# Kernel tuning notes

Hardware: AMD Instinct MI355X
Metric: run time of the kernel (lower is better)

The kernel has to match this reference:

```python
import jax, jax.numpy as jnp
import numpy as np

N_A, N_B = 50000, 20000   # authors, teams
E0, E1, E2 = 600000, 300000, 300000  # coauthor(A->A), writes(A->B), influences(B->A)
D = 128                   # in_feats = out_feats


def setup_inputs() -> dict:
    key = jax.random.key(0)
    ks = jax.random.split(key, 12)
    h_A = jax.random.normal(ks[0], (N_A, D), jnp.float32)
    h_B = jax.random.normal(ks[1], (N_B, D), jnp.float32)
    W0 = jax.random.normal(ks[2], (D, D), jnp.float32) * 0.05
    W1 = jax.random.normal(ks[3], (D, D), jnp.float32) * 0.05
    W2 = jax.random.normal(ks[4], (D, D), jnp.float32) * 0.05
    b0 = jnp.zeros((D,), jnp.float32)
    b1 = jnp.zeros((D,), jnp.float32)
    b2 = jnp.zeros((D,), jnp.float32)
    src0 = jax.random.randint(ks[5], (E0,), 0, N_A)
    dst0 = jax.random.randint(ks[6], (E0,), 0, N_A)
    src1 = jax.random.randint(ks[7], (E1,), 0, N_A)
    dst1 = jax.random.randint(ks[8], (E1,), 0, N_B)
    src2 = jax.random.randint(ks[9], (E2,), 0, N_B)
    dst2 = jax.random.randint(ks[10], (E2,), 0, N_A)
    return dict(h_A=h_A, h_B=h_B, W0=W0, b0=b0, W1=W1, b1=b1, W2=W2, b2=b2,
                src0=src0, dst0=dst0, src1=src1, dst1=dst1, src2=src2, dst2=dst2)


def _graph_conv(x_src, W, b, src, dst, n_dst):
    """DGL GraphConv, norm='both': out = D_dst^{-1/2} A D_src^{-1/2} (X W) + b."""
    n_src = x_src.shape[0]
    ones = jnp.ones(src.shape[0], x_src.dtype)
    deg_out = jnp.clip(jax.ops.segment_sum(ones, src, num_segments=n_src), 1.0)
    deg_in = jnp.clip(jax.ops.segment_sum(ones, dst, num_segments=n_dst), 1.0)
    m = (x_src @ W) * (deg_out ** -0.5)[:, None]          # [n_src, D]
    agg = jax.ops.segment_sum(m[src], dst, num_segments=n_dst)  # [n_dst, D]
    return agg * (deg_in ** -0.5)[:, None] + b


def reference(h_A, h_B, W0, b0, W1, b1, W2, b2, src0, dst0, src1, dst1, src2, dst2):
    # HeteroGraphConv(aggregate='sum'): sum per-relation GraphConv outputs per dst ntype.
    out_A = (_graph_conv(h_A, W0, b0, src0, dst0, N_A)
             + _graph_conv(h_B, W2, b2, src2, dst2, N_A))
    out_B = _graph_conv(h_A, W1, b1, src1, dst1, N_B)
    # every ntype present in h receives an output, so no passthrough branch fires
    return out_A, out_B
```

## Files before the change

kernel.cpp:

```cpp
#include <hip/hip_runtime.h>

#define NA 50000
#define NB 20000
#define NE0 600000
#define NE1 300000
#define NE2 300000
#define DD 128
#define SUB 32768
#define PER 18750
#define PSUB 8192


typedef short bf16x8 __attribute__((ext_vector_type(8)));
typedef float f32x4 __attribute__((ext_vector_type(4)));

__device__ __forceinline__ unsigned short f2bf(float f) {
    union { float f; unsigned int u; } v; v.f = f;
    unsigned int r = v.u + 0x7fffu + ((v.u >> 16) & 1u);
    return (unsigned short)(r >> 16);
}
__device__ __forceinline__ float lo2f(unsigned int u) {
    union { float f; unsigned int u; } v; v.u = u << 16;
    return v.f;
}
__device__ __forceinline__ float hi2f(unsigned int u) {
    union { float f; unsigned int u; } v; v.u = u & 0xffff0000u;
    return v.f;
}

__global__ __launch_bounds__(1024) void hist_kernel(
    const int* __restrict__ s0, const int* __restrict__ d0,
    const int* __restrict__ s1, const int* __restrict__ d1,
    const int* __restrict__ s2, const int* __restrict__ d2,
    unsigned int* __restrict__ Pd,
    const float* __restrict__ W0, const float* __restrict__ W1,
    const float* __restrict__ W2, unsigned short* __restrict__ Wt)
{
    __shared__ unsigned int h32[SUB / 2];
    const int cfg = blockIdx.z;
    if (cfg == 6) {
        int flat = blockIdx.y * 2 + blockIdx.x;
        if (flat >= 48) return;
        int i = flat * 1024 + threadIdx.x;
        int w = i >> 14, r = i & (DD * DD - 1);
        int c = r >> 7, k = r & (DD - 1);
        const float* W = (w == 0) ? W0 : ((w == 1) ? W1 : W2);
        Wt[i] = f2bf(W[k * DD + c]);
        return;
    }
    const int En[6] = {NE0, NE0, NE1, NE1, NE2, NE2};
    const int Kn[6] = {NA, NA, NA, NB, NB, NA};
    const int Gn[6] = {32, 32, 16, 16, 16, 16};
    const int Po[6] = {0, 1600000, 3200000, 4000000, 4320000, 4640000};
    int E = En[cfg], K = Kn[cfg], G = Gn[cfg];
    int sub = blockIdx.x, g = blockIdx.y;
    int nsub = (K + SUB - 1) / SUB;
    if (sub >= nsub || g >= G) return;
    const int* keys = cfg == 0 ? s0 : cfg == 1 ? d0 : cfg == 2 ? s1
                    : cfg == 3 ? d1 : cfg == 4 ? s2 : d2;
    int lo = sub * SUB;
    int hi = min(K, lo + SUB);
    int cnt = hi - lo;
    for (int i = threadIdx.x; i < SUB / 2; i += 1024) h32[i] = 0;
    __syncthreads();
    int e1 = min(E, g * PER + PER);
    for (int e = g * PER + threadIdx.x; e < e1; e += 1024) {
        int k = keys[e];
        if (k >= lo && k < hi) {
            int kk = k - lo;
            atomicAdd(&h32[kk >> 1], 1u << ((kk & 1) << 4));
        }
    }
    __syncthreads();
    unsigned int* outp = Pd + ((Po[cfg] + g * K + lo) >> 1);
    for (int i = threadIdx.x; i < cnt / 2; i += 1024) outp[i] = h32[i];
}

__global__ __launch_bounds__(256) void reduce2(
    const unsigned short* __restrict__ P16, int* __restrict__ ideg,
    float* __restrict__ rdeg, int* __restrict__ spart,
    unsigned char* __restrict__ cum8)
{
    __shared__ int lds[256];
    const int y = blockIdx.y;
    const int Ro[6] = {0, NA, 2 * NA, 3 * NA, 3 * NA + NB, 3 * NA + 2 * NB};
    const int Kr[6] = {NA, NA, NA, NB, NB, NA};
    const int Gr[6] = {32, 32, 16, 16, 16, 16};
    const int Po[6] = {0, 1600000, 3200000, 4000000, 4320000, 4640000};
    const int Co[6] = {0, 0, 0, 1600000, 0, 1920000};
    int K = Kr[y], G = Gr[y];
    int b = blockIdx.x, t = threadIdx.x;
    int nchunk = (K + 255) >> 8;
    if (b >= nchunk) return;
    int key = b * 256 + t;
    bool valid = key < K;
    bool din = (y == 1) || (y == 3) || (y == 5);
    const unsigned short* p = P16 + Po[y] + key;
    unsigned char* cb = cum8 + Co[y] + key;
    int run = 0;
    for (int g = 0; g < G; ++g) {
        if (din && valid) cb[g * K] = (unsigned char)run;
        run += valid ? p[g * K] : 0;
    }
    if (valid) {
        ideg[Ro[y] + key] = run;
        rdeg[Ro[y] + key] = rsqrtf(fmaxf((float)run, 1.f));
    }
    if (din) {
        int slot = (y - 1) >> 1;
        lds[t] = run; __syncthreads();
        for (int o = 128; o > 0; o >>= 1) {
            if (t < o) lds[t] += lds[t + o];
            __syncthreads();
        }
        if (t == 0) spart[slot * 256 + b] = lds[0];
    }
}

__global__ __launch_bounds__(256) void scan3(
    const int* __restrict__ ideg, const int* __restrict__ spart,
    int* __restrict__ rp)
{
    __shared__ int lds[256];
    const int y = blockIdx.y;
    const int off[3] = {NA, 3 * NA, 3 * NA + 2 * NB};
    const int nn[3]  = {NA, NB, NA};
    const int ro[3]  = {0, NA, NA + NB};
    int n = nn[y];
    int b = blockIdx.x, t = threadIdx.x;
    if (b * 1024 >= n) return;

    lds[t] = (t < 4 * b) ? spart[y * 256 + t] : 0;
    __syncthreads();
    for (int o = 128; o > 0; o >>= 1) {
        if (t < o) lds[t] += lds[t + o];
        __syncthreads();
    }
    int pv = lds[0];
    __syncthreads();

    const int* deg = ideg + off[y];
    int base = b * 1024 + t * 4;
    int v[4]; int tsum = 0;
    #pragma unroll
    for (int k = 0; k < 4; ++k) {
        v[k] = (base + k < n) ? deg[base + k] : 0;
        tsum += v[k];
    }
    lds[t] = tsum; __syncthreads();
    for (int o = 1; o < 256; o <<= 1) {
        int x = (t >= o) ? lds[t - o] : 0;
        __syncthreads();
        lds[t] += x;
        __syncthreads();
    }
    int run = lds[t] - tsum + pv;
    int* rowptr = rp + ro[y];
    #pragma unroll
    for (int k = 0; k < 4; ++k) {
        if (base + k < n) rowptr[base + k] = run;
        run += v[k];
    }
}

__global__ __launch_bounds__(512) void work_kernel(
    const int* __restrict__ s0, const int* __restrict__ d0,
    const int* __restrict__ s1, const int* __restrict__ d1,
    const int* __restrict__ s2, const int* __restrict__ d2,
    const unsigned char* __restrict__ cum8, const int* __restrict__ rp,
    unsigned short* __restrict__ csr0, unsigned short* __restrict__ csr1,
    unsigned short* __restrict__ csr2,
    const float* __restrict__ hA, const float* __restrict__ hB,
    const unsigned short* __restrict__ Wt, const float* __restrict__ rdeg,
    unsigned short* __restrict__ mA0, unsigned short* __restrict__ mA1,
    unsigned short* __restrict__ mB2)
{
    __shared__ int cnt_lds[PSUB];
    int bx = blockIdx.x;
    int wid  = threadIdx.x >> 6;
    int lane = threadIdx.x & 63;
    int quad = lane >> 4;
    int l16  = lane & 15;
    if (bx < 391) {
        int base = bx * 128 + wid * 16;
        if (base >= NA) return;
        int arow = base + l16;
        if (arow >= NA) arow = NA - 1;
        bf16x8 a[4];
        #pragma unroll
        for (int kk = 0; kk < 4; ++kk) {
            const float4* p = (const float4*)(hA + (size_t)arow * DD + kk * 32 + quad * 8);
            float4 u = p[0], w = p[1];
            bf16x8 t;
            t[0] = (short)f2bf(u.x); t[1] = (short)f2bf(u.y);
            t[2] = (short)f2bf(u.z); t[3] = (short)f2bf(u.w);
            t[4] = (short)f2bf(w.x); t[5] = (short)f2bf(w.y);
            t[6] = (short)f2bf(w.z); t[7] = (short)f2bf(w.w);
            a[kk] = t;
        }
        float rs0[4], rs1[4]; int orow0 = base + quad * 4;
        #pragma unroll
        for (int r = 0; r < 4; ++r) {
            int orow = orow0 + r; int c = orow < NA ? orow : 0;
            rs0[r] = rdeg[c]; rs1[r] = rdeg[2 * NA + c];
        }
        #pragma unroll
        for (int ct = 0; ct < 8; ++ct) {
            f32x4 acc0 = {0.f, 0.f, 0.f, 0.f};
            f32x4 acc1 = {0.f, 0.f, 0.f, 0.f};
            const unsigned short* wp = Wt + (size_t)(ct * 16 + l16) * DD + quad * 8;
            #pragma unroll
            for (int kk = 0; kk < 4; ++kk) {
                bf16x8 b0 = *(const bf16x8*)(wp + kk * 32);
                bf16x8 b1 = *(const bf16x8*)(wp + 16384 + kk * 32);
                acc0 = __builtin_amdgcn_mfma_f32_16x16x32_bf16(a[kk], b0, acc0, 0, 0, 0);
                acc1 = __builtin_amdgcn_mfma_f32_16x16x32_bf16(a[kk], b1, acc1, 0, 0, 0);
            }
            #pragma unroll
            for (int r = 0; r < 4; ++r) {
                int orow = orow0 + r;
                if (orow < NA) {
                    mA0[(size_t)orow * DD + ct * 16 + l16] = f2bf(acc0[r] * rs0[r]);
                    mA1[(size_t)orow * DD + ct * 16 + l16] = f2bf(acc1[r] * rs1[r]);
                }
            }
        }
        return;
    }
    if (bx < 548) {
        int base = (bx - 391) * 128 + wid * 16;
        if (base >= NB) return;
        int arow = base + l16;
        if (arow >= NB) arow = NB - 1;
        bf16x8 a[4];
        #pragma unroll
        for (int kk = 0; kk < 4; ++kk) {
            const float4* p = (const float4*)(hB + (size_t)arow * DD + kk * 32 + quad * 8);
            float4 u = p[0], w = p[1];
            bf16x8 t;
            t[0] = (short)f2bf(u.x); t[1] = (short)f2bf(u.y);
            t[2] = (short)f2bf(u.z); t[3] = (short)f2bf(u.w);
            t[4] = (short)f2bf(w.x); t[5] = (short)f2bf(w.y);
            t[6] = (short)f2bf(w.z); t[7] = (short)f2bf(w.w);
            a[kk] = t;
        }
        float rs[4]; int orow0 = base + quad * 4;
        #pragma unroll
        for (int r = 0; r < 4; ++r) {
            int orow = orow0 + r;
            rs[r] = rdeg[3 * NA + NB + (orow < NB ? orow : 0)];
        }
        #pragma unroll
        for (int ct = 0; ct < 8; ++ct) {
            f32x4 acc = {0.f, 0.f, 0.f, 0.f};
            const unsigned short* wp = Wt + 32768 + (size_t)(ct * 16 + l16) * DD + quad * 8;
            #pragma unroll
            for (int kk = 0; kk < 4; ++kk) {
                bf16x8 b = *(const bf16x8*)(wp + kk * 32);
                acc = __builtin_amdgcn_mfma_f32_16x16x32_bf16(a[kk], b, acc, 0, 0, 0);
            }
            #pragma unroll
            for (int r = 0; r < 4; ++r) {
                int orow = orow0 + r;
                if (orow < NB)
                    mB2[(size_t)orow * DD + ct * 16 + l16] = f2bf(acc[r] * rs[r]);
            }
        }
        return;
    }
    int pb = bx - 548;
    int z, g, sub;
    if (pb < 224)      { z = 0; g = pb / 7;          sub = pb % 7; }
    else if (pb < 272) { z = 1; g = (pb - 224) / 3;  sub = (pb - 224) % 3; }
    else               { z = 2; g = (pb - 272) / 7;  sub = (pb - 272) % 7; }
    const int En[3] = {NE0, NE1, NE2};
    const int Kn[3] = {NA, NB, NA};
    const int Co[3] = {0, 1600000, 1920000};
    const int ro[3] = {0, NA, NA + NB};
    int E = En[z], K = Kn[z];
    const int* src = z == 0 ? s0 : z == 1 ? s1 : s2;
    const int* dst = z == 0 ? d0 : z == 1 ? d1 : d2;
    unsigned short* csr = z == 0 ? csr0 : z == 1 ? csr1 : csr2;
    int lo = sub * PSUB;
    int hi = min(K, lo + PSUB);
    int cnt = hi - lo;
    const int* rpz = rp + ro[z] + lo;
    const unsigned char* cz = cum8 + Co[z] + (size_t)g * K + lo;
    for (int i = threadIdx.x; i < cnt; i += 512)
        cnt_lds[i] = rpz[i] + (int)cz[i];
    __syncthreads();
    int e1 = min(E, g * PER + PER);
    for (int e = g * PER + threadIdx.x; e < e1; e += 512) {
        int d = dst[e];
        if (d >= lo && d < hi) {
            int pos = atomicAdd(&cnt_lds[d - lo], 1);
            csr[pos] = (unsigned short)src[e];
        }
    }
}

__device__ __forceinline__ void acc8(float* o, uint4 u) {
    o[0] += lo2f(u.x); o[1] += hi2f(u.x);
    o[2] += lo2f(u.y); o[3] += hi2f(u.y);
    o[4] += lo2f(u.z); o[5] += hi2f(u.z);
    o[6] += lo2f(u.w); o[7] += hi2f(u.w);
}
__device__ __forceinline__ void gather_rel4(
    const char* __restrict__ Mb, const unsigned short* __restrict__ csr,
    int st, int n, int lane, int q, unsigned laneoff, float* o)
{
    for (int ch = 0; ch < n; ch += 64) {
        int m = n - ch; if (m > 64) m = 64;
        int idx = csr[st + ch + (lane < m ? lane : m - 1)];
        int j = 0;
        for (; j + 8 <= m; j += 8) {
            int sA = __shfl(idx, j + q);
            int sB = __shfl(idx, j + 4 + q);
            uint4 uA = *(const uint4*)(Mb + (((unsigned)sA << 8) + laneoff));
            uint4 uB = *(const uint4*)(Mb + (((unsigned)sB << 8) + laneoff));
            acc8(o, uA); acc8(o, uB);
        }
        if (j + 4 <= m) {
            int s = __shfl(idx, j + q);
            uint4 u = *(const uint4*)(Mb + (((unsigned)s << 8) + laneoff));
            acc8(o, u);
            j += 4;
        }
        if (j < m) {
            int jj = j + q;
            float w = jj < m ? 1.f : 0.f;
            int s = __shfl(idx, jj < m ? jj : m - 1);
            uint4 u = *(const uint4*)(Mb + (((unsigned)s << 8) + laneoff));
            o[0] = fmaf(w, lo2f(u.x), o[0]); o[1] = fmaf(w, hi2f(u.x), o[1]);
            o[2] = fmaf(w, lo2f(u.y), o[2]); o[3] = fmaf(w, hi2f(u.y), o[3]);
            o[4] = fmaf(w, lo2f(u.z), o[4]); o[5] = fmaf(w, hi2f(u.z), o[5]);
            o[6] = fmaf(w, lo2f(u.w), o[6]); o[7] = fmaf(w, hi2f(u.w), o[7]);
        }
    }
}

__global__ __launch_bounds__(256) void gather_all(
    const unsigned short* __restrict__ mA0, const unsigned short* __restrict__ mA1,
    const unsigned short* __restrict__ mB2,
    const unsigned short* __restrict__ csr0, const unsigned short* __restrict__ csr1,
    const unsigned short* __restrict__ csr2,
    const int* __restrict__ rp, const int* __restrict__ ideg,
    const float* __restrict__ rdeg,
    const float* __restrict__ b0, const float* __restrict__ b1,
    const float* __restrict__ b2,
    float* __restrict__ out)
{
    int wid = threadIdx.x >> 6, lane = threadIdx.x & 63;
    int q = lane >> 4, l16 = lane & 15;
    unsigned laneoff = (unsigned)l16 * 16u;
    float v[8];
    #pragma unroll
    for (int i = 0; i < 8; ++i) v[i] = 0.f;
    float* op;
    const float *bia, *bib;

    if (blockIdx.x < 12500) {
        int d = blockIdx.x * 4 + wid;
        float c[8];
        #pragma unroll
        for (int i = 0; i < 8; ++i) c[i] = 0.f;
        gather_rel4((const char*)mA0, csr0, rp[d], ideg[NA + d], lane, q, laneoff, v);
        gather_rel4((const char*)mB2, csr2, rp[NA + NB + d], ideg[3 * NA + 2 * NB + d],
                    lane, q, laneoff, c);
        float r0 = rdeg[NA + d], r2 = rdeg[3 * NA + 2 * NB + d];
        #pragma unroll
        for (int i = 0; i < 8; ++i) v[i] = v[i] * r0 + c[i] * r2;
        op = out + (size_t)d * DD;
        bia = b0; bib = b2;
    } else {
        int d = (blockIdx.x - 12500) * 4 + wid;
        gather_rel4((const char*)mA1, csr1, rp[NA + d], ideg[3 * NA + d],
                    lane, q, laneoff, v);
        float r1 = rdeg[3 * NA + d];
        #pragma unroll
        for (int i = 0; i < 8; ++i) v[i] *= r1;
        op = out + (size_t)(NA + d) * DD;
        bia = b1; bib = 0;
    }

    #pragma unroll
    for (int i = 0; i < 8; ++i) {
        v[i] += __shfl_down(v[i], 32);
        v[i] += __shfl_down(v[i], 16);
    }
    if (lane < 16) {
        int col = l16 * 8;
        float4 ba0 = *(const float4*)(bia + col);
        float4 ba1 = *(const float4*)(bia + col + 4);
        if (bib) {
            float4 bb0 = *(const float4*)(bib + col);
            float4 bb1 = *(const float4*)(bib + col + 4);
            ba0.x += bb0.x; ba0.y += bb0.y; ba0.z += bb0.z; ba0.w += bb0.w;
            ba1.x += bb1.x; ba1.y += bb1.y; ba1.z += bb1.z; ba1.w += bb1.w;
        }
        float4 o0 = {v[0] + ba0.x, v[1] + ba0.y, v[2] + ba0.z, v[3] + ba0.w};
        float4 o1 = {v[4] + ba1.x, v[5] + ba1.y, v[6] + ba1.z, v[7] + ba1.w};
        *(float4*)(op + col) = o0;
        *(float4*)(op + col + 4) = o1;
    }
}

extern "C" void kernel_launch(void* const* d_in, const int* in_sizes, int n_in,
                              void* d_out, int out_size, void* d_ws, size_t ws_size,
                              hipStream_t stream) {
    const float* hA = (const float*)d_in[0];
    const float* hB = (const float*)d_in[1];
    const float* W0 = (const float*)d_in[2];
    const float* b0 = (const float*)d_in[3];
    const float* W1 = (const float*)d_in[4];
    const float* b1 = (const float*)d_in[5];
    const float* W2 = (const float*)d_in[6];
    const float* b2 = (const float*)d_in[7];
    const int* s0 = (const int*)d_in[8];
    const int* d0 = (const int*)d_in[9];
    const int* s1 = (const int*)d_in[10];
    const int* d1 = (const int*)d_in[11];
    const int* s2 = (const int*)d_in[12];
    const int* d2 = (const int*)d_in[13];
    float* out = (float*)d_out;
    char* ws = (char*)d_ws;

    unsigned short* mA0 = (unsigned short*)(ws + 0);
    unsigned short* mA1 = (unsigned short*)(ws + 12800000);
    unsigned short* mB2 = (unsigned short*)(ws + 25600000);
    unsigned short* P16 = (unsigned short*)(ws + 0);
    unsigned int*   Pd  = (unsigned int*)(ws + 0);
    unsigned short* Wt  = (unsigned short*)(ws + 30720000);
    float* rdeg         = (float*)(ws + 30818304);
    int*   ideg         = (int*)  (ws + 31778304);
    int*   rp           = (int*)  (ws + 32738304);
    int*   spart        = (int*)  (ws + 33218304);
    unsigned char* cum8 = (unsigned char*)(ws + 33221376);
    unsigned short* csr0= (unsigned short*)(ws + 35941376);
    unsigned short* csr1= (unsigned short*)(ws + 37141376);
    unsigned short* csr2= (unsigned short*)(ws + 37741376);

    hist_kernel<<<dim3(2, 32, 7), 1024, 0, stream>>>(s0, d0, s1, d1, s2, d2,
        Pd, W0, W1, W2, Wt);
    reduce2<<<dim3(196, 6), 256, 0, stream>>>(P16, ideg, rdeg, spart, cum8);
    scan3<<<dim3(49, 3), 256, 0, stream>>>(ideg, spart, rp);
    work_kernel<<<548 + 384, 512, 0, stream>>>(s0, d0, s1, d1, s2, d2,
        cum8, rp, csr0, csr1, csr2,
        hA, hB, Wt, rdeg, mA0, mA1, mB2);
    gather_all<<<12500 + 5000, 256, 0, stream>>>(mA0, mA1, mB2,
        csr0, csr1, csr2, rp, ideg, rdeg, b0, b1, b2, out);
}
```

Measured before the change: 243.1 us.

## Build degrees and CSR with global atomics instead of LDS partial histograms

Replaces the LDS-privatized partial histograms and the per-group cumulative offset table (hist_kernel, reduce2, cum8) with direct global atomicAdd degree counting over all edges, after a small zeroing kernel. The CSR fill now takes a per-row cursor, initialised from the row pointers in scan3, and claims slots with global atomics. This removes the repeated edge scans per key subrange and the large partial-count buffers. In exchange it relies on global atomic throughput and makes the order of neighbours within each CSR row nondeterministic.

```diff
diff --git a/kernel.cpp b/kernel.cpp
--- a/kernel.cpp
+++ b/kernel.cpp
@@ -6,9 +6,6 @@
 #define NE1 300000
 #define NE2 300000
 #define DD 128
-#define SUB 32768
-#define PER 18750
-#define PSUB 8192
 
 
 typedef short bf16x8 __attribute__((ext_vector_type(8)));
@@ -28,98 +25,79 @@
     return v.f;
 }
 
-__global__ __launch_bounds__(1024) void hist_kernel(
+__global__ __launch_bounds__(1024) void zero_k(int4* __restrict__ idegv)
+{
+    int i = blockIdx.x * 1024 + threadIdx.x;
+    if (i < 60000) { int4 z = {0, 0, 0, 0}; idegv[i] = z; }
+}
+
+__global__ __launch_bounds__(1024) void degwt_k(
     const int* __restrict__ s0, const int* __restrict__ d0,
     const int* __restrict__ s1, const int* __restrict__ d1,
     const int* __restrict__ s2, const int* __restrict__ d2,
-    unsigned int* __restrict__ Pd,
+    int* __restrict__ ideg,
     const float* __restrict__ W0, const float* __restrict__ W1,
     const float* __restrict__ W2, unsigned short* __restrict__ Wt)
 {
-    __shared__ unsigned int h32[SUB / 2];
-    const int cfg = blockIdx.z;
-    if (cfg == 6) {
-        int flat = blockIdx.y * 2 + blockIdx.x;
-        if (flat >= 48) return;
-        int i = flat * 1024 + threadIdx.x;
+    int bx = blockIdx.x;
+    if (bx < 48) {
+        int i = bx * 1024 + threadIdx.x;
         int w = i >> 14, r = i & (DD * DD - 1);
         int c = r >> 7, k = r & (DD - 1);
         const float* W = (w == 0) ? W0 : ((w == 1) ? W1 : W2);
         Wt[i] = f2bf(W[k * DD + c]);
         return;
     }
-    const int En[6] = {NE0, NE0, NE1, NE1, NE2, NE2};
-    const int Kn[6] = {NA, NA, NA, NB, NB, NA};
-    const int Gn[6] = {32, 32, 16, 16, 16, 16};
-    const int Po[6] = {0, 1600000, 3200000, 4000000, 4320000, 4640000};
-    int E = En[cfg], K = Kn[cfg], G = Gn[cfg];
-    int sub = blockIdx.x, g = blockIdx.y;
-    int nsub = (K + SUB - 1) / SUB;
-    if (sub >= nsub || g >= G) return;
-    const int* keys = cfg == 0 ? s0 : cfg == 1 ? d0 : cfg == 2 ? s1
-                    : cfg == 3 ? d1 : cfg == 4 ? s2 : d2;
-    int lo = sub * SUB;
-    int hi = min(K, lo + SUB);
-    int cnt = hi - lo;
-    for (int i = threadIdx.x; i < SUB / 2; i += 1024) h32[i] = 0;
+    int pb = bx - 48;
+    int z = (pb < 293) ? 0 : (pb < 440) ? 1 : 2;
+    const int zb[3] = {0, 293, 440};
+    const int En[3] = {NE0, NE1, NE2};
+    const int so[3] = {0, 2 * NA, 3 * NA + NB};
+    const int di[3] = {NA, 3 * NA, 3 * NA + 2 * NB};
+    int E = En[z];
+    const int* src = z == 0 ? s0 : z == 1 ? s1 : s2;
+    const int* dst = z == 0 ? d0 : z == 1 ? d1 : d2;
+    int e0 = (pb - zb[z]) * 2048 + threadIdx.x;
+    #pragma unroll
+    for (int j = 0; j < 2; ++j) {
+        int e = e0 + j * 1024;
+        if (e < E) {
+            int s = src[e], d = dst[e];
+            atomicAdd(&ideg[so[z] + s], 1);
+            atomicAdd(&ideg[di[z] + d], 1);
+        }
+    }
+}
+
+__global__ __launch_bounds__(256) void rsp_k(
+    const int* __restrict__ ideg, float* __restrict__ rdeg,
+    int* __restrict__ spart)
+{
+    int y = blockIdx.y, b = blockIdx.x, t = threadIdx.x;
+    if (y == 0) {
+        int i = b * 256 + t;
+        if (i < 4 * NA + 2 * NB) rdeg[i] = rsqrtf(fmaxf((float)ideg[i], 1.f));
+        return;
+    }
+    __shared__ int lds[256];
+    const int segb[3] = {NA, 3 * NA, 3 * NA + 2 * NB};
+    const int segn[3] = {NA, NB, NA};
+    int s = y - 1;
+    int n = segn[s];
+    if (b * 256 >= n) return;
+    int key = b * 256 + t;
+    lds[t] = (key < n) ? ideg[segb[s] + key] : 0;
     __syncthreads();
-    int e1 = min(E, g * PER + PER);
-    for (int e = g * PER + threadIdx.x; e < e1; e += 1024) {
-        int k = keys[e];
-        if (k >= lo && k < hi) {
-            int kk = k - lo;
-            atomicAdd(&h32[kk >> 1], 1u << ((kk & 1) << 4));
-        }
-    }
-    __syncthreads();
-    unsigned int* outp = Pd + ((Po[cfg] + g * K + lo) >> 1);
-    for (int i = threadIdx.x; i < cnt / 2; i += 1024) outp[i] = h32[i];
-}
-
-__global__ __launch_bounds__(256) void reduce2(
-    const unsigned short* __restrict__ P16, int* __restrict__ ideg,
-    float* __restrict__ rdeg, int* __restrict__ spart,
-    unsigned char* __restrict__ cum8)
-{
-    __shared__ int lds[256];
-    const int y = blockIdx.y;
-    const int Ro[6] = {0, NA, 2 * NA, 3 * NA, 3 * NA + NB, 3 * NA + 2 * NB};
-    const int Kr[6] = {NA, NA, NA, NB, NB, NA};
-    const int Gr[6] = {32, 32, 16, 16, 16, 16};
-    const int Po[6] = {0, 1600000, 3200000, 4000000, 4320000, 4640000};
-    const int Co[6] = {0, 0, 0, 1600000, 0, 1920000};
-    int K = Kr[y], G = Gr[y];
-    int b = blockIdx.x, t = threadIdx.x;
-    int nchunk = (K + 255) >> 8;
-    if (b >= nchunk) return;
-    int key = b * 256 + t;
-    bool valid = key < K;
-    bool din = (y == 1) || (y == 3) || (y == 5);
-    const unsigned short* p = P16 + Po[y] + key;
-    unsigned char* cb = cum8 + Co[y] + key;
-    int run = 0;
-    for (int g = 0; g < G; ++g) {
-        if (din && valid) cb[g * K] = (unsigned char)run;
-        run += valid ? p[g * K] : 0;
-    }
-    if (valid) {
-        ideg[Ro[y] + key] = run;
-        rdeg[Ro[y] + key] = rsqrtf(fmaxf((float)run, 1.f));
-    }
-    if (din) {
-        int slot = (y - 1) >> 1;
-        lds[t] = run; __syncthreads();
-        for (int o = 128; o > 0; o >>= 1) {
-            if (t < o) lds[t] += lds[t + o];
-            __syncthreads();
-        }
-        if (t == 0) spart[slot * 256 + b] = lds[0];
-    }
+    for (int o = 128; o > 0; o >>= 1) {
+        if (t < o) lds[t] += lds[t + o];
+        __syncthreads();
+    }
+    if (t == 0) spart[s * 256 + b] = lds[0];
 }
 
 __global__ __launch_bounds__(256) void scan3(
     const int* __restrict__ ideg, const int* __restrict__ spart,
-    int* __restrict__ rp)
+    int* __restrict__ rp, int* __restrict__ cursor)
 {
     __shared__ int lds[256];
     const int y = blockIdx.y;
@@ -156,9 +134,10 @@
     }
     int run = lds[t] - tsum + pv;
     int* rowptr = rp + ro[y];
+    int* cur = cursor + ro[y];
     #pragma unroll
     for (int k = 0; k < 4; ++k) {
-        if (base + k < n) rowptr[base + k] = run;
+        if (base + k < n) { rowptr[base + k] = run; cur[base + k] = run; }
         run += v[k];
     }
 }
@@ -167,7 +146,7 @@
     const int* __restrict__ s0, const int* __restrict__ d0,
     const int* __restrict__ s1, const int* __restrict__ d1,
     const int* __restrict__ s2, const int* __restrict__ d2,
-    const unsigned char* __restrict__ cum8, const int* __restrict__ rp,
+    int* __restrict__ cursor,
     unsigned short* __restrict__ csr0, unsigned short* __restrict__ csr1,
     unsigned short* __restrict__ csr2,
     const float* __restrict__ hA, const float* __restrict__ hB,
@@ -175,7 +154,6 @@
     unsigned short* __restrict__ mA0, unsigned short* __restrict__ mA1,
     unsigned short* __restrict__ mB2)
 {
-    __shared__ int cnt_lds[PSUB];
     int bx = blockIdx.x;
     int wid  = threadIdx.x >> 6;
     int lane = threadIdx.x & 63;
@@ -269,34 +247,28 @@
         return;
     }
     int pb = bx - 548;
-    int z, g, sub;
-    if (pb < 224)      { z = 0; g = pb / 7;          sub = pb % 7; }
-    else if (pb < 272) { z = 1; g = (pb - 224) / 3;  sub = (pb - 224) % 3; }
-    else               { z = 2; g = (pb - 272) / 7;  sub = (pb - 272) % 7; }
+    int z = (pb < 586) ? 0 : (pb < 879) ? 1 : 2;
+    const int zb[3] = {0, 586, 879};
     const int En[3] = {NE0, NE1, NE2};
-    const int Kn[3] = {NA, NB, NA};
-    const int Co[3] = {0, 1600000, 1920000};
     const int ro[3] = {0, NA, NA + NB};
-    int E = En[z], K = Kn[z];
+    int E = En[z];
     const int* src = z == 0 ? s0 : z == 1 ? s1 : s2;
     const int* dst = z == 0 ? d0 : z == 1 ? d1 : d2;
     unsigned short* csr = z == 0 ? csr0 : z == 1 ? csr1 : csr2;
-    int lo = sub * PSUB;
-    int hi = min(K, lo + PSUB);
-    int cnt = hi - lo;
-    const int* rpz = rp + ro[z] + lo;
-    const unsigned char* cz = cum8 + Co[z] + (size_t)g * K + lo;
-    for (int i = threadIdx.x; i < cnt; i += 512)
-        cnt_lds[i] = rpz[i] + (int)cz[i];
-    __syncthreads();
-    int e1 = min(E, g * PER + PER);
-    for (int e = g * PER + threadIdx.x; e < e1; e += 512) {
-        int d = dst[e];
-        if (d >= lo && d < hi) {
-            int pos = atomicAdd(&cnt_lds[d - lo], 1);
-            csr[pos] = (unsigned short)src[e];
-        }
-    }
+    int* cur = cursor + ro[z];
+    int e0 = (pb - zb[z]) * 1024 + threadIdx.x;
+    int e1 = e0 + 512;
+    bool v0 = e0 < E, v1 = e1 < E;
+    int ce0 = v0 ? e0 : 0, ce1 = v1 ? e1 : 0;
+    int d_0 = dst[ce0];
+    int d_1 = dst[ce1];
+    int s_0 = src[ce0];
+    int s_1 = src[ce1];
+    int p0 = 0, p1 = 0;
+    if (v0) p0 = atomicAdd(&cur[d_0], 1);
+    if (v1) p1 = atomicAdd(&cur[d_1], 1);
+    if (v0) csr[p0] = (unsigned short)s_0;
+    if (v1) csr[p1] = (unsigned short)s_1;
 }
 
 __device__ __forceinline__ void acc8(float* o, uint4 u) {
@@ -428,24 +400,23 @@
     unsigned short* mA0 = (unsigned short*)(ws + 0);
     unsigned short* mA1 = (unsigned short*)(ws + 12800000);
     unsigned short* mB2 = (unsigned short*)(ws + 25600000);
-    unsigned short* P16 = (unsigned short*)(ws + 0);
-    unsigned int*   Pd  = (unsigned int*)(ws + 0);
     unsigned short* Wt  = (unsigned short*)(ws + 30720000);
     float* rdeg         = (float*)(ws + 30818304);
     int*   ideg         = (int*)  (ws + 31778304);
     int*   rp           = (int*)  (ws + 32738304);
     int*   spart        = (int*)  (ws + 33218304);
-    unsigned char* cum8 = (unsigned char*)(ws + 33221376);
+    int*   cursor       = (int*)  (ws + 33221376);
     unsigned short* csr0= (unsigned short*)(ws + 35941376);
     unsigned short* csr1= (unsigned short*)(ws + 37141376);
     unsigned short* csr2= (unsigned short*)(ws + 37741376);
 
-    hist_kernel<<<dim3(2, 32, 7), 1024, 0, stream>>>(s0, d0, s1, d1, s2, d2,
-        Pd, W0, W1, W2, Wt);
-    reduce2<<<dim3(196, 6), 256, 0, stream>>>(P16, ideg, rdeg, spart, cum8);
-    scan3<<<dim3(49, 3), 256, 0, stream>>>(ideg, spart, rp);
-    work_kernel<<<548 + 384, 512, 0, stream>>>(s0, d0, s1, d1, s2, d2,
-        cum8, rp, csr0, csr1, csr2,
+    zero_k<<<59, 1024, 0, stream>>>((int4*)ideg);
+    degwt_k<<<48 + 293 + 147 + 147, 1024, 0, stream>>>(s0, d0, s1, d1, s2, d2,
+        ideg, W0, W1, W2, Wt);
+    rsp_k<<<dim3(938, 4), 256, 0, stream>>>(ideg, rdeg, spart);
+    scan3<<<dim3(49, 3), 256, 0, stream>>>(ideg, spart, rp, cursor);
+    work_kernel<<<548 + 1172, 512, 0, stream>>>(s0, d0, s1, d1, s2, d2,
+        cursor, csr0, csr1, csr2,
         hA, hB, Wt, rdeg, mA0, mA1, mB2);
     gather_all<<<12500 + 5000, 256, 0, stream>>>(mA0, mA1, mB2,
         csr0, csr1, csr2, rp, ideg, rdeg, b0, b1, b2, out);
```

Result: slower. 331.0 us (+36.1%).
